# Kernel tuning notes

Measured on AMD Instinct MI355X. Metric: run time of the kernel, lower is better.

The kernel has to match this reference:

```python
import jax, jax.numpy as jnp
import numpy as np

N, F, H, G = 4096, 256, 8, 128  # atoms, filters, heads, groups
D = F // H  # head dim = 32


def setup_inputs() -> dict:
    key = jax.random.key(0)
    ks = jax.random.split(key, 12)
    x = jax.random.normal(ks[0], (N, F), dtype=jnp.float32)
    # sorted group ids in [0, G): block_diag over unique-count blocks == equality mask on sorted ids
    seg = jnp.sort(jax.random.randint(ks[1], (N,), 0, G, dtype=jnp.int32))
    elem_index = jnp.stack([jnp.arange(N, dtype=jnp.int32), seg])  # [2, N]
    s = 1.0 / np.sqrt(F)
    def lin(k):
        kw, kb = jax.random.split(k)
        return (jax.random.normal(kw, (F, F), dtype=jnp.float32) * s,
                jnp.zeros((F,), dtype=jnp.float32))
    Wq, bq = lin(ks[2]); Wk, bk = lin(ks[3]); Wv, bv = lin(ks[4])
    Wo1, bo1 = lin(ks[5]); Wo2, bo2 = lin(ks[6])
    return {"x": x, "elem_index": elem_index,
            "Wq": Wq, "bq": bq, "Wk": Wk, "bk": bk, "Wv": Wv, "bv": bv,
            "Wo1": Wo1, "bo1": bo1, "Wo2": Wo2, "bo2": bo2}


def reference(x, elem_index, Wq, bq, Wk, bk, Wv, bv, Wo1, bo1, Wo2, bo2):
    n = x.shape[0]
    # projections -> [H, N, D]
    q = (x @ Wq.T + bq).reshape(n, H, D).transpose(1, 0, 2)
    k = (x @ Wk.T + bk).reshape(n, H, D).transpose(1, 0, 2)
    v = (x @ Wv.T + bv).reshape(n, H, D).transpose(1, 0, 2)
    attn = jnp.einsum('hnd,hmd->hnm', q, k)          # [H, N, N]
    attn = jax.nn.silu(attn)                          # attn_act = activation() in source
    seg = elem_index[1]
    mask = (seg[:, None] == seg[None, :]).astype(attn.dtype)  # block-diagonal (sorted ids)
    attn = attn * mask
    out = jnp.einsum('hnm,hmd->hnd', attn, v)        # [H, N, D]
    out = out.transpose(1, 0, 2).reshape(n, F)       # [N, F]
    out = out @ Wo1.T + bo1
    out = jax.ops.segment_sum(out, seg, num_segments=G)  # scatter sum by group -> [G, F]
    out = out @ Wo2.T + bo2
    return jax.nn.silu(out)
```

## Files before the change

kernel.cpp:

```cpp
#include <hip/hip_runtime.h>
#include <math.h>

#define NATOMS 4096
#define FDIM   256
#define NHEAD  8
#define DHEAD  32
#define NGRP   128

typedef __bf16 bf16x8 __attribute__((ext_vector_type(8)));
typedef float  floatx4 __attribute__((ext_vector_type(4)));
typedef unsigned short u16x4 __attribute__((ext_vector_type(4)));

__device__ __forceinline__ float silu_f(float x) {
    return x / (1.0f + __expf(-x));
}

__device__ __forceinline__ unsigned short f2bf(float f) {
    union { float f; unsigned int u; } a;
    a.f = f;
    unsigned int r = a.u + 0x7FFF + ((a.u >> 16) & 1);
    return (unsigned short)(r >> 16);
}

__global__ __launch_bounds__(256) void prep_kernel(
    const float* __restrict__ x,
    const float* __restrict__ Wq, const float* __restrict__ Wk, const float* __restrict__ Wv,
    const float* __restrict__ bq, const float* __restrict__ bk, const float* __restrict__ bv,
    const int* __restrict__ seg,
    unsigned short* __restrict__ xb, unsigned short* __restrict__ Wb,
    float* __restrict__ b_all, int* __restrict__ off, float* __restrict__ cntf)
{
    int tid = threadIdx.x;
    unsigned int u = blockIdx.x * 256 + tid;

    if (blockIdx.x == 0 && tid < NGRP) {
        int g = tid;
        auto lb = [&](int val) {
            int lo = 0, hi = NATOMS;
            while (lo < hi) {
                int mid = (lo + hi) >> 1;
                if (seg[mid] < val) lo = mid + 1; else hi = mid;
            }
            return lo;
        };
        int a = lb(g);
        int b = lb(g + 1);
        off[g] = a;
        if (g == NGRP - 1) off[NGRP] = NATOMS;
        cntf[g] = (float)(b - a);
    }
    if (blockIdx.x == 1 && tid < 192) {
        const float* src = (tid < 64) ? bq : (tid < 128) ? bk : bv;
        int t = tid & 63;
        ((float4*)b_all)[tid] = ((const float4*)src)[t];
    }

    const unsigned int NX4 = 262144;
    const unsigned int NW4 = 16384;
    float4 fv;
    u16x4* dst;
    if (u < NX4) {
        fv = ((const float4*)x)[u];
        dst = (u16x4*)xb + u;
    } else {
        unsigned int r = u - NX4;
        unsigned int w = r / NW4;
        unsigned int i = r - w * NW4;
        const float* W = (w == 0) ? Wq : (w == 1) ? Wk : Wv;
        fv = ((const float4*)W)[i];
        dst = (u16x4*)Wb + (size_t)w * NW4 + i;
    }
    u16x4 o;
    o[0] = f2bf(fv.x); o[1] = f2bf(fv.y); o[2] = f2bf(fv.z); o[3] = f2bf(fv.w);
    *dst = o;
}

__global__ __launch_bounds__(256) void qkv_mfma(
    const unsigned short* __restrict__ xb, const unsigned short* __restrict__ Wb,
    const float* __restrict__ b_all, float* __restrict__ qkv)
{
    int tid = threadIdx.x;
    int lane = tid & 63;
    int ww = tid >> 6;
    int wrow = ww >> 1, wcol = ww & 1;
    int m_base = blockIdx.x * 64 + wrow * 32;
    int n_base = blockIdx.y * 128 + wcol * 64;

    int l15 = lane & 15;
    int quad = lane >> 4;
    int kq = quad * 8;

    floatx4 acc[2][4] = {};

    const unsigned short* arow0 = xb + (size_t)(m_base + l15) * 256 + kq;
    const unsigned short* arow1 = arow0 + 16 * 256;
    const unsigned short* brow[4];
#pragma unroll
    for (int ni = 0; ni < 4; ++ni)
        brow[ni] = Wb + (size_t)(n_base + ni * 16 + l15) * 256 + kq;

#pragma unroll
    for (int ks = 0; ks < 8; ++ks) {
        int ko = ks * 32;
        bf16x8 a0 = *(const bf16x8*)(arow0 + ko);
        bf16x8 a1 = *(const bf16x8*)(arow1 + ko);
#pragma unroll
        for (int ni = 0; ni < 4; ++ni) {
            bf16x8 b = *(const bf16x8*)(brow[ni] + ko);
            acc[0][ni] = __builtin_amdgcn_mfma_f32_16x16x32_bf16(a0, b, acc[0][ni], 0, 0, 0);
            acc[1][ni] = __builtin_amdgcn_mfma_f32_16x16x32_bf16(a1, b, acc[1][ni], 0, 0, 0);
        }
    }

#pragma unroll
    for (int mi = 0; mi < 2; ++mi) {
#pragma unroll
        for (int ni = 0; ni < 4; ++ni) {
            int col_g = n_base + ni * 16 + l15;
            int w = col_g >> 8, c = col_g & 255;
            float bias = b_all[col_g];
            float* outp = qkv + (size_t)w * (NATOMS * FDIM) + c;
#pragma unroll
            for (int r = 0; r < 4; ++r) {
                int row = m_base + mi * 16 + quad * 4 + r;
                outp[(size_t)row * FDIM] = acc[mi][ni][r] + bias;
            }
        }
    }
}

__global__ __launch_bounds__(256) void gemm_small(
    const float* __restrict__ A, const float* __restrict__ B,
    const float* __restrict__ bias, const float* __restrict__ rowScale,
    float* __restrict__ C, int M, int Ncols, int K, int act)
{
    __shared__ float As[32][36];
    __shared__ float Bs[32][36];

    int tid = threadIdx.x;
    int bm = blockIdx.y * 32;
    int bn = blockIdx.x * 32;
    int tx = tid & 15;
    int ty = tid >> 4;
    int lm = tid >> 3;
    int lk = (tid & 7) << 2;

    float acc[2][2] = {};

    for (int kt = 0; kt < K; kt += 32) {
        const float4 av = *(const float4*)(A + (size_t)(bm + lm) * K + kt + lk);
        const float4 bv = *(const float4*)(B + (size_t)(bn + lm) * K + kt + lk);
        As[lk + 0][lm] = av.x; As[lk + 1][lm] = av.y;
        As[lk + 2][lm] = av.z; As[lk + 3][lm] = av.w;
        Bs[lk + 0][lm] = bv.x; Bs[lk + 1][lm] = bv.y;
        Bs[lk + 2][lm] = bv.z; Bs[lk + 3][lm] = bv.w;
        __syncthreads();

#pragma unroll
        for (int kk = 0; kk < 32; ++kk) {
            float a0 = As[kk][ty * 2], a1 = As[kk][ty * 2 + 1];
            float c0 = Bs[kk][tx * 2], c1 = Bs[kk][tx * 2 + 1];
            acc[0][0] = fmaf(a0, c0, acc[0][0]);
            acc[0][1] = fmaf(a0, c1, acc[0][1]);
            acc[1][0] = fmaf(a1, c0, acc[1][0]);
            acc[1][1] = fmaf(a1, c1, acc[1][1]);
        }
        __syncthreads();
    }

#pragma unroll
    for (int i = 0; i < 2; ++i) {
        int m = bm + ty * 2 + i;
        float rs = rowScale ? rowScale[m] : 1.0f;
#pragma unroll
        for (int j = 0; j < 2; ++j) {
            int n = bn + tx * 2 + j;
            float vv = acc[i][j] + rs * bias[n];
            if (act) vv = silu_f(vv);
            C[(size_t)m * Ncols + n] = vv;
        }
    }
}

#define JT 32
#define IT 64

__global__ __launch_bounds__(256) void attn_kernel(
    const float* __restrict__ q, const float* __restrict__ k,
    const float* __restrict__ v, const int* __restrict__ off,
    float* __restrict__ Ysum)
{
    int g = blockIdx.x, h = blockIdx.y;
    int base = off[g];
    int end  = off[g + 1];
    base = min(max(base, 0), NATOMS);
    end  = min(max(end, base), NATOMS);
    int n = end - base;

    __shared__ float4 qt4[IT * 8];
    __shared__ float4 vt4[JT * 8];
    __shared__ float  wred[8][JT];
    __shared__ float  w[JT];
    __shared__ float  red[8][DHEAD];

    int tid = threadIdx.x;
    int jj = tid & 31;
    int iq = tid >> 5;
    int d = tid & 31;
    int r = tid >> 5;

    const float4* q4 = (const float4*)(q + (size_t)base * FDIM) + h * 8;
    const float4* k4 = (const float4*)(k + (size_t)base * FDIM) + h * 8;
    const float4* v4 = (const float4*)(v + (size_t)base * FDIM) + h * 8;

    float accY = 0.0f;

    for (int j0 = 0; j0 < n; j0 += JT) {
        int jt_n = min(JT, n - j0);
        __syncthreads();
        for (int idx = tid; idx < jt_n * 8; idx += 256)
            vt4[idx] = v4[(size_t)(j0 + (idx >> 3)) * 64 + (idx & 7)];

        float4 kr[8];
        {
            int jrow = (jj < jt_n) ? (j0 + jj) : j0;
#pragma unroll
            for (int c = 0; c < 8; ++c) kr[c] = k4[(size_t)jrow * 64 + c];
        }

        float wpart = 0.0f;
        for (int i0 = 0; i0 < n; i0 += IT) {
            int it_n = min(IT, n - i0);
            __syncthreads();
            for (int idx = tid; idx < it_n * 8; idx += 256)
                qt4[idx] = q4[(size_t)(i0 + (idx >> 3)) * 64 + (idx & 7)];
            __syncthreads();
            if (jj < jt_n) {
                for (int ii = iq; ii < it_n; ii += 8) {
                    const float4* qr = &qt4[ii * 8];
                    float s = 0.0f;
#pragma unroll
                    for (int c = 0; c < 8; ++c) {
                        float4 a = qr[c];
                        s = fmaf(a.x, kr[c].x, s);
                        s = fmaf(a.y, kr[c].y, s);
                        s = fmaf(a.z, kr[c].z, s);
                        s = fmaf(a.w, kr[c].w, s);
                    }
                    wpart += silu_f(s);
                }
            }
        }
        wred[iq][jj] = wpart;
        __syncthreads();
        if (tid < JT) {
            float s = 0.0f;
#pragma unroll
            for (int rr = 0; rr < 8; ++rr) s += wred[rr][tid];
            w[tid] = s;
        }
        __syncthreads();
        const float* vts = (const float*)vt4;
        for (int j = r; j < jt_n; j += 8)
            accY = fmaf(w[j], vts[j * 32 + d], accY);
    }

    red[r][d] = accY;
    __syncthreads();
    if (r == 0) {
        float s = 0.0f;
#pragma unroll
        for (int rr = 0; rr < 8; ++rr) s += red[rr][d];
        Ysum[(size_t)g * FDIM + h * DHEAD + d] = s;
    }
}

extern "C" void kernel_launch(void* const* d_in, const int* in_sizes, int n_in,
                              void* d_out, int out_size, void* d_ws, size_t ws_size,
                              hipStream_t stream) {
    const float* x    = (const float*)d_in[0];
    const int*   eidx = (const int*)  d_in[1];
    const float* Wq   = (const float*)d_in[2];
    const float* bq   = (const float*)d_in[3];
    const float* Wk   = (const float*)d_in[4];
    const float* bk   = (const float*)d_in[5];
    const float* Wv   = (const float*)d_in[6];
    const float* bv   = (const float*)d_in[7];
    const float* Wo1  = (const float*)d_in[8];
    const float* bo1  = (const float*)d_in[9];
    const float* Wo2  = (const float*)d_in[10];
    const float* bo2  = (const float*)d_in[11];
    float* out = (float*)d_out;

    const int* seg = eidx + NATOMS;

    const size_t NF = (size_t)NATOMS * FDIM;
    const size_t GF = (size_t)NGRP * FDIM;

    float* q     = (float*)d_ws;
    float* k     = q + NF;
    float* v     = k + NF;
    float* Ysum  = v + NF;
    float* S     = Ysum + GF;
    float* cntf  = S + GF;
    float* b_all = cntf + NGRP;
    int*   off   = (int*)(b_all + 768);
    unsigned short* xb = (unsigned short*)((float*)off + 160);
    unsigned short* Wb = xb + NF;

    prep_kernel<<<1216, 256, 0, stream>>>(x, Wq, Wk, Wv, bq, bk, bv, seg,
                                          xb, Wb, b_all, off, cntf);

    dim3 gproj(NATOMS / 64, 768 / 128);
    qkv_mfma<<<gproj, 256, 0, stream>>>(xb, Wb, b_all, q);

    dim3 gattn(NGRP, NHEAD);
    attn_kernel<<<gattn, 256, 0, stream>>>(q, k, v, off, Ysum);

    dim3 gsmall(FDIM / 32, NGRP / 32);
    gemm_small<<<gsmall, 256, 0, stream>>>(Ysum, Wo1, bo1, cntf, S, NGRP, FDIM, FDIM, 0);

    gemm_small<<<gsmall, 256, 0, stream>>>(S, Wo2, bo2, nullptr, out, NGRP, FDIM, FDIM, 1);
}
```

Before: 128.2 us.

## Fuse all stages into one persistent cooperative kernel with grid syncs

Replaces the five separate launches (prep/convert, QKV MFMA GEMM, attention, two small GEMMs) with a single cooperative kernel of 256 blocks that loops over each stage's work and uses grid.sync between stages. This removes per-launch overhead and the separate bias-gather buffer, since biases are now read directly. In exchange, attention runs as 4 serial (group, head) jobs per block instead of 1024 concurrent blocks, which lowers occupancy and latency hiding. It also adds grid-wide barrier costs, and the QKV phase spreads 384 tiles unevenly over 256 blocks.

```diff
diff --git a/kernel.cpp b/kernel.cpp
--- a/kernel.cpp
+++ b/kernel.cpp
@@ -1,11 +1,15 @@
 #include <hip/hip_runtime.h>
+#include <hip/hip_cooperative_groups.h>
 #include <math.h>
+
+namespace cg = cooperative_groups;
 
 #define NATOMS 4096
 #define FDIM   256
 #define NHEAD  8
 #define DHEAD  32
 #define NGRP   128
+#define NBLK   256
 
 typedef __bf16 bf16x8 __attribute__((ext_vector_type(8)));
 typedef float  floatx4 __attribute__((ext_vector_type(4)));
@@ -22,18 +26,91 @@
     return (unsigned short)(r >> 16);
 }
 
-__global__ __launch_bounds__(256) void prep_kernel(
-    const float* __restrict__ x,
+struct SharedMem {
+    union {
+        struct {
+            float4 qt4[64 * 8];
+            float4 vt4[32 * 8];
+            float  wred[8][32];
+            float  w[32];
+            float  red[8][32];
+        } a;
+        struct {
+            float As[32][36];
+            float Bs[32][36];
+        } g;
+    };
+};
+
+__device__ void gemm32_body(SharedMem& sm,
+                            const float* __restrict__ A, const float* __restrict__ B,
+                            const float* __restrict__ bias, const float* __restrict__ rowScale,
+                            float* __restrict__ C, int act, int blk)
+{
+    const int K = FDIM, Ncols = FDIM;
+    int tid = threadIdx.x;
+    int bm = (blk >> 3) * 32;
+    int bn = (blk & 7) * 32;
+    int tx = tid & 15;
+    int ty = tid >> 4;
+    int lm = tid >> 3;
+    int lk = (tid & 7) << 2;
+
+    float acc[2][2] = {};
+
+    for (int kt = 0; kt < K; kt += 32) {
+        const float4 av = *(const float4*)(A + (size_t)(bm + lm) * K + kt + lk);
+        const float4 bv = *(const float4*)(B + (size_t)(bn + lm) * K + kt + lk);
+        sm.g.As[lk + 0][lm] = av.x; sm.g.As[lk + 1][lm] = av.y;
+        sm.g.As[lk + 2][lm] = av.z; sm.g.As[lk + 3][lm] = av.w;
+        sm.g.Bs[lk + 0][lm] = bv.x; sm.g.Bs[lk + 1][lm] = bv.y;
+        sm.g.Bs[lk + 2][lm] = bv.z; sm.g.Bs[lk + 3][lm] = bv.w;
+        __syncthreads();
+
+#pragma unroll
+        for (int kk = 0; kk < 32; ++kk) {
+            float a0 = sm.g.As[kk][ty * 2], a1 = sm.g.As[kk][ty * 2 + 1];
+            float c0 = sm.g.Bs[kk][tx * 2], c1 = sm.g.Bs[kk][tx * 2 + 1];
+            acc[0][0] = fmaf(a0, c0, acc[0][0]);
+            acc[0][1] = fmaf(a0, c1, acc[0][1]);
+            acc[1][0] = fmaf(a1, c0, acc[1][0]);
+            acc[1][1] = fmaf(a1, c1, acc[1][1]);
+        }
+        __syncthreads();
+    }
+
+#pragma unroll
+    for (int i = 0; i < 2; ++i) {
+        int m = bm + ty * 2 + i;
+        float rs = rowScale ? rowScale[m] : 1.0f;
+#pragma unroll
+        for (int j = 0; j < 2; ++j) {
+            int n = bn + tx * 2 + j;
+            float vv = acc[i][j] + rs * bias[n];
+            if (act) vv = silu_f(vv);
+            C[(size_t)m * Ncols + n] = vv;
+        }
+    }
+}
+
+__global__ __launch_bounds__(256) void mega_kernel(
+    const float* __restrict__ x, const int* __restrict__ seg,
     const float* __restrict__ Wq, const float* __restrict__ Wk, const float* __restrict__ Wv,
     const float* __restrict__ bq, const float* __restrict__ bk, const float* __restrict__ bv,
-    const int* __restrict__ seg,
+    const float* __restrict__ Wo1, const float* __restrict__ bo1,
+    const float* __restrict__ Wo2, const float* __restrict__ bo2,
+    float* __restrict__ out,
     unsigned short* __restrict__ xb, unsigned short* __restrict__ Wb,
-    float* __restrict__ b_all, int* __restrict__ off, float* __restrict__ cntf)
+    float* __restrict__ qkv, float* __restrict__ Ysum, float* __restrict__ S,
+    float* __restrict__ cntf, int* __restrict__ off)
 {
-    int tid = threadIdx.x;
-    unsigned int u = blockIdx.x * 256 + tid;
-
-    if (blockIdx.x == 0 && tid < NGRP) {
+    cg::grid_group grid = cg::this_grid();
+    __shared__ SharedMem sm;
+
+    const int tid = threadIdx.x;
+    const int bid = blockIdx.x;
+
+    if (bid == 0 && tid < NGRP) {
         int g = tid;
         auto lb = [&](int val) {
             int lo = 0, hi = NATOMS;
@@ -49,230 +126,179 @@
         if (g == NGRP - 1) off[NGRP] = NATOMS;
         cntf[g] = (float)(b - a);
     }
-    if (blockIdx.x == 1 && tid < 192) {
-        const float* src = (tid < 64) ? bq : (tid < 128) ? bk : bv;
-        int t = tid & 63;
-        ((float4*)b_all)[tid] = ((const float4*)src)[t];
-    }
 
     const unsigned int NX4 = 262144;
     const unsigned int NW4 = 16384;
-    float4 fv;
-    u16x4* dst;
-    if (u < NX4) {
-        fv = ((const float4*)x)[u];
-        dst = (u16x4*)xb + u;
-    } else {
-        unsigned int r = u - NX4;
-        unsigned int w = r / NW4;
-        unsigned int i = r - w * NW4;
-        const float* W = (w == 0) ? Wq : (w == 1) ? Wk : Wv;
-        fv = ((const float4*)W)[i];
-        dst = (u16x4*)Wb + (size_t)w * NW4 + i;
-    }
-    u16x4 o;
-    o[0] = f2bf(fv.x); o[1] = f2bf(fv.y); o[2] = f2bf(fv.z); o[3] = f2bf(fv.w);
-    *dst = o;
-}
-
-__global__ __launch_bounds__(256) void qkv_mfma(
-    const unsigned short* __restrict__ xb, const unsigned short* __restrict__ Wb,
-    const float* __restrict__ b_all, float* __restrict__ qkv)
-{
-    int tid = threadIdx.x;
-    int lane = tid & 63;
-    int ww = tid >> 6;
-    int wrow = ww >> 1, wcol = ww & 1;
-    int m_base = blockIdx.x * 64 + wrow * 32;
-    int n_base = blockIdx.y * 128 + wcol * 64;
-
-    int l15 = lane & 15;
-    int quad = lane >> 4;
-    int kq = quad * 8;
-
-    floatx4 acc[2][4] = {};
-
-    const unsigned short* arow0 = xb + (size_t)(m_base + l15) * 256 + kq;
-    const unsigned short* arow1 = arow0 + 16 * 256;
-    const unsigned short* brow[4];
-#pragma unroll
-    for (int ni = 0; ni < 4; ++ni)
-        brow[ni] = Wb + (size_t)(n_base + ni * 16 + l15) * 256 + kq;
-
-#pragma unroll
-    for (int ks = 0; ks < 8; ++ks) {
-        int ko = ks * 32;
-        bf16x8 a0 = *(const bf16x8*)(arow0 + ko);
-        bf16x8 a1 = *(const bf16x8*)(arow1 + ko);
-#pragma unroll
-        for (int ni = 0; ni < 4; ++ni) {
-            bf16x8 b = *(const bf16x8*)(brow[ni] + ko);
-            acc[0][ni] = __builtin_amdgcn_mfma_f32_16x16x32_bf16(a0, b, acc[0][ni], 0, 0, 0);
-            acc[1][ni] = __builtin_amdgcn_mfma_f32_16x16x32_bf16(a1, b, acc[1][ni], 0, 0, 0);
-        }
-    }
-
-#pragma unroll
-    for (int mi = 0; mi < 2; ++mi) {
-#pragma unroll
-        for (int ni = 0; ni < 4; ++ni) {
-            int col_g = n_base + ni * 16 + l15;
-            int w = col_g >> 8, c = col_g & 255;
-            float bias = b_all[col_g];
-            float* outp = qkv + (size_t)w * (NATOMS * FDIM) + c;
-#pragma unroll
-            for (int r = 0; r < 4; ++r) {
-                int row = m_base + mi * 16 + quad * 4 + r;
-                outp[(size_t)row * FDIM] = acc[mi][ni][r] + bias;
-            }
-        }
-    }
-}
-
-__global__ __launch_bounds__(256) void gemm_small(
-    const float* __restrict__ A, const float* __restrict__ B,
-    const float* __restrict__ bias, const float* __restrict__ rowScale,
-    float* __restrict__ C, int M, int Ncols, int K, int act)
-{
-    __shared__ float As[32][36];
-    __shared__ float Bs[32][36];
-
-    int tid = threadIdx.x;
-    int bm = blockIdx.y * 32;
-    int bn = blockIdx.x * 32;
-    int tx = tid & 15;
-    int ty = tid >> 4;
-    int lm = tid >> 3;
-    int lk = (tid & 7) << 2;
-
-    float acc[2][2] = {};
-
-    for (int kt = 0; kt < K; kt += 32) {
-        const float4 av = *(const float4*)(A + (size_t)(bm + lm) * K + kt + lk);
-        const float4 bv = *(const float4*)(B + (size_t)(bn + lm) * K + kt + lk);
-        As[lk + 0][lm] = av.x; As[lk + 1][lm] = av.y;
-        As[lk + 2][lm] = av.z; As[lk + 3][lm] = av.w;
-        Bs[lk + 0][lm] = bv.x; Bs[lk + 1][lm] = bv.y;
-        Bs[lk + 2][lm] = bv.z; Bs[lk + 3][lm] = bv.w;
-        __syncthreads();
-
-#pragma unroll
-        for (int kk = 0; kk < 32; ++kk) {
-            float a0 = As[kk][ty * 2], a1 = As[kk][ty * 2 + 1];
-            float c0 = Bs[kk][tx * 2], c1 = Bs[kk][tx * 2 + 1];
-            acc[0][0] = fmaf(a0, c0, acc[0][0]);
-            acc[0][1] = fmaf(a0, c1, acc[0][1]);
-            acc[1][0] = fmaf(a1, c0, acc[1][0]);
-            acc[1][1] = fmaf(a1, c1, acc[1][1]);
-        }
-        __syncthreads();
-    }
-
-#pragma unroll
-    for (int i = 0; i < 2; ++i) {
-        int m = bm + ty * 2 + i;
-        float rs = rowScale ? rowScale[m] : 1.0f;
-#pragma unroll
-        for (int j = 0; j < 2; ++j) {
-            int n = bn + tx * 2 + j;
-            float vv = acc[i][j] + rs * bias[n];
-            if (act) vv = silu_f(vv);
-            C[(size_t)m * Ncols + n] = vv;
-        }
-    }
-}
-
-#define JT 32
-#define IT 64
-
-__global__ __launch_bounds__(256) void attn_kernel(
-    const float* __restrict__ q, const float* __restrict__ k,
-    const float* __restrict__ v, const int* __restrict__ off,
-    float* __restrict__ Ysum)
-{
-    int g = blockIdx.x, h = blockIdx.y;
-    int base = off[g];
-    int end  = off[g + 1];
-    base = min(max(base, 0), NATOMS);
-    end  = min(max(end, base), NATOMS);
-    int n = end - base;
-
-    __shared__ float4 qt4[IT * 8];
-    __shared__ float4 vt4[JT * 8];
-    __shared__ float  wred[8][JT];
-    __shared__ float  w[JT];
-    __shared__ float  red[8][DHEAD];
-
-    int tid = threadIdx.x;
-    int jj = tid & 31;
-    int iq = tid >> 5;
-    int d = tid & 31;
-    int r = tid >> 5;
-
-    const float4* q4 = (const float4*)(q + (size_t)base * FDIM) + h * 8;
-    const float4* k4 = (const float4*)(k + (size_t)base * FDIM) + h * 8;
-    const float4* v4 = (const float4*)(v + (size_t)base * FDIM) + h * 8;
-
-    float accY = 0.0f;
-
-    for (int j0 = 0; j0 < n; j0 += JT) {
-        int jt_n = min(JT, n - j0);
-        __syncthreads();
-        for (int idx = tid; idx < jt_n * 8; idx += 256)
-            vt4[idx] = v4[(size_t)(j0 + (idx >> 3)) * 64 + (idx & 7)];
-
-        float4 kr[8];
-        {
-            int jrow = (jj < jt_n) ? (j0 + jj) : j0;
-#pragma unroll
-            for (int c = 0; c < 8; ++c) kr[c] = k4[(size_t)jrow * 64 + c];
-        }
-
-        float wpart = 0.0f;
-        for (int i0 = 0; i0 < n; i0 += IT) {
-            int it_n = min(IT, n - i0);
+    const unsigned int NTOT = NX4 + 3 * NW4;
+    for (unsigned int u = bid * 256u + tid; u < NTOT; u += NBLK * 256u) {
+        float4 fv;
+        u16x4* dst;
+        if (u < NX4) {
+            fv = ((const float4*)x)[u];
+            dst = (u16x4*)xb + u;
+        } else {
+            unsigned int r = u - NX4;
+            unsigned int w = r / NW4;
+            unsigned int i = r - w * NW4;
+            const float* W = (w == 0) ? Wq : (w == 1) ? Wk : Wv;
+            fv = ((const float4*)W)[i];
+            dst = (u16x4*)Wb + (size_t)w * NW4 + i;
+        }
+        u16x4 o;
+        o[0] = f2bf(fv.x); o[1] = f2bf(fv.y); o[2] = f2bf(fv.z); o[3] = f2bf(fv.w);
+        *dst = o;
+    }
+    grid.sync();
+
+    {
+        int lane = tid & 63;
+        int ww = tid >> 6;
+        int wrow = ww >> 1, wcol = ww & 1;
+        int l15 = lane & 15;
+        int quad = lane >> 4;
+        int kq = quad * 8;
+
+        for (int job = bid; job < 384; job += NBLK) {
+            int tm = job & 63;
+            int tn = job >> 6;
+            int m_base = tm * 64 + wrow * 32;
+            int n_base = tn * 128 + wcol * 64;
+
+            floatx4 acc[2][4] = {};
+
+            const unsigned short* arow0 = xb + (size_t)(m_base + l15) * 256 + kq;
+            const unsigned short* arow1 = arow0 + 16 * 256;
+            const unsigned short* brow[4];
+#pragma unroll
+            for (int ni = 0; ni < 4; ++ni)
+                brow[ni] = Wb + (size_t)(n_base + ni * 16 + l15) * 256 + kq;
+
+#pragma unroll
+            for (int ks = 0; ks < 8; ++ks) {
+                int ko = ks * 32;
+                bf16x8 a0 = *(const bf16x8*)(arow0 + ko);
+                bf16x8 a1 = *(const bf16x8*)(arow1 + ko);
+#pragma unroll
+                for (int ni = 0; ni < 4; ++ni) {
+                    bf16x8 b = *(const bf16x8*)(brow[ni] + ko);
+                    acc[0][ni] = __builtin_amdgcn_mfma_f32_16x16x32_bf16(a0, b, acc[0][ni], 0, 0, 0);
+                    acc[1][ni] = __builtin_amdgcn_mfma_f32_16x16x32_bf16(a1, b, acc[1][ni], 0, 0, 0);
+                }
+            }
+
+#pragma unroll
+            for (int mi = 0; mi < 2; ++mi) {
+#pragma unroll
+                for (int ni = 0; ni < 4; ++ni) {
+                    int col_g = n_base + ni * 16 + l15;
+                    int w = col_g >> 8, c = col_g & 255;
+                    const float* bptr = (w == 0) ? bq : (w == 1) ? bk : bv;
+                    float bias = bptr[c];
+                    float* outp = qkv + (size_t)w * ((size_t)NATOMS * FDIM) + c;
+#pragma unroll
+                    for (int r = 0; r < 4; ++r) {
+                        int row = m_base + mi * 16 + quad * 4 + r;
+                        outp[(size_t)row * FDIM] = acc[mi][ni][r] + bias;
+                    }
+                }
+            }
+        }
+    }
+    grid.sync();
+
+    {
+        const float* q = qkv;
+        const float* k = qkv + (size_t)NATOMS * FDIM;
+        const float* v = qkv + 2 * (size_t)NATOMS * FDIM;
+
+        int jj = tid & 31;
+        int iq = tid >> 5;
+        int d = tid & 31;
+        int r = tid >> 5;
+
+        for (int t = 0; t < 4; ++t) {
+            int job = bid * 4 + t;
+            int g = job >> 3, h = job & 7;
+
+            int base = off[g];
+            int end  = off[g + 1];
+            base = min(max(base, 0), NATOMS);
+            end  = min(max(end, base), NATOMS);
+            int n = end - base;
+
+            const float4* q4 = (const float4*)(q + (size_t)base * FDIM) + h * 8;
+            const float4* k4 = (const float4*)(k + (size_t)base * FDIM) + h * 8;
+            const float4* v4 = (const float4*)(v + (size_t)base * FDIM) + h * 8;
+
+            float accY = 0.0f;
+
+            for (int j0 = 0; j0 < n; j0 += 32) {
+                int jt_n = min(32, n - j0);
+                __syncthreads();
+                for (int idx = tid; idx < jt_n * 8; idx += 256)
+                    sm.a.vt4[idx] = v4[(size_t)(j0 + (idx >> 3)) * 64 + (idx & 7)];
+
+                float4 kr[8];
+                {
+                    int jrow = (jj < jt_n) ? (j0 + jj) : j0;
+#pragma unroll
+                    for (int c = 0; c < 8; ++c) kr[c] = k4[(size_t)jrow * 64 + c];
+                }
+
+                float wpart = 0.0f;
+                for (int i0 = 0; i0 < n; i0 += 64) {
+                    int it_n = min(64, n - i0);
+                    __syncthreads();
+                    for (int idx = tid; idx < it_n * 8; idx += 256)
+                        sm.a.qt4[idx] = q4[(size_t)(i0 + (idx >> 3)) * 64 + (idx & 7)];
+                    __syncthreads();
+                    if (jj < jt_n) {
+                        for (int ii = iq; ii < it_n; ii += 8) {
+                            const float4* qr = &sm.a.qt4[ii * 8];
+                            float s = 0.0f;
+#pragma unroll
+                            for (int c = 0; c < 8; ++c) {
+                                float4 a = qr[c];
+                                s = fmaf(a.x, kr[c].x, s);
+                                s = fmaf(a.y, kr[c].y, s);
+                                s = fmaf(a.z, kr[c].z, s);
+                                s = fmaf(a.w, kr[c].w, s);
+                            }
+                            wpart += silu_f(s);
+                        }
+                    }
+                }
+                sm.a.wred[iq][jj] = wpart;
+                __syncthreads();
+                if (tid < 32) {
+                    float s = 0.0f;
+#pragma unroll
+                    for (int rr = 0; rr < 8; ++rr) s += sm.a.wred[rr][tid];
+                    sm.a.w[tid] = s;
+                }
+                __syncthreads();
+                const float* vts = (const float*)sm.a.vt4;
+                for (int j = r; j < jt_n; j += 8)
+                    accY = fmaf(sm.a.w[j], vts[j * 32 + d], accY);
+            }
+
+            sm.a.red[r][d] = accY;
             __syncthreads();
-            for (int idx = tid; idx < it_n * 8; idx += 256)
-                qt4[idx] = q4[(size_t)(i0 + (idx >> 3)) * 64 + (idx & 7)];
+            if (r == 0) {
+                float s = 0.0f;
+#pragma unroll
+                for (int rr = 0; rr < 8; ++rr) s += sm.a.red[rr][d];
+                Ysum[(size_t)g * FDIM + h * DHEAD + d] = s;
+            }
             __syncthreads();
-            if (jj < jt_n) {
-                for (int ii = iq; ii < it_n; ii += 8) {
-                    const float4* qr = &qt4[ii * 8];
-                    float s = 0.0f;
-#pragma unroll
-                    for (int c = 0; c < 8; ++c) {
-                        float4 a = qr[c];
-                        s = fmaf(a.x, kr[c].x, s);
-                        s = fmaf(a.y, kr[c].y, s);
-                        s = fmaf(a.z, kr[c].z, s);
-                        s = fmaf(a.w, kr[c].w, s);
-                    }
-                    wpart += silu_f(s);
-                }
-            }
-        }
-        wred[iq][jj] = wpart;
-        __syncthreads();
-        if (tid < JT) {
-            float s = 0.0f;
-#pragma unroll
-            for (int rr = 0; rr < 8; ++rr) s += wred[rr][tid];
-            w[tid] = s;
-        }
-        __syncthreads();
-        const float* vts = (const float*)vt4;
-        for (int j = r; j < jt_n; j += 8)
-            accY = fmaf(w[j], vts[j * 32 + d], accY);
-    }
-
-    red[r][d] = accY;
-    __syncthreads();
-    if (r == 0) {
-        float s = 0.0f;
-#pragma unroll
-        for (int rr = 0; rr < 8; ++rr) s += red[rr][d];
-        Ysum[(size_t)g * FDIM + h * DHEAD + d] = s;
-    }
+        }
+    }
+    grid.sync();
+
+    if (bid < 32) gemm32_body(sm, Ysum, Wo1, bo1, cntf, S, 0, bid);
+    grid.sync();
+
+    if (bid < 32) gemm32_body(sm, S, Wo2, bo2, nullptr, out, 1, bid);
 }
 
 extern "C" void kernel_launch(void* const* d_in, const int* in_sizes, int n_in,
@@ -297,28 +323,24 @@
     const size_t NF = (size_t)NATOMS * FDIM;
     const size_t GF = (size_t)NGRP * FDIM;
 
-    float* q     = (float*)d_ws;
-    float* k     = q + NF;
-    float* v     = k + NF;
-    float* Ysum  = v + NF;
+    float* qkv   = (float*)d_ws;
+    float* Ysum  = qkv + 3 * NF;
     float* S     = Ysum + GF;
     float* cntf  = S + GF;
-    float* b_all = cntf + NGRP;
-    int*   off   = (int*)(b_all + 768);
+    int*   off   = (int*)(cntf + NGRP);
     unsigned short* xb = (unsigned short*)((float*)off + 160);
     unsigned short* Wb = xb + NF;
 
-    prep_kernel<<<1216, 256, 0, stream>>>(x, Wq, Wk, Wv, bq, bk, bv, seg,
-                                          xb, Wb, b_all, off, cntf);
-
-    dim3 gproj(NATOMS / 64, 768 / 128);
-    qkv_mfma<<<gproj, 256, 0, stream>>>(xb, Wb, b_all, q);
-
-    dim3 gattn(NGRP, NHEAD);
-    attn_kernel<<<gattn, 256, 0, stream>>>(q, k, v, off, Ysum);
-
-    dim3 gsmall(FDIM / 32, NGRP / 32);
-    gemm_small<<<gsmall, 256, 0, stream>>>(Ysum, Wo1, bo1, cntf, S, NGRP, FDIM, FDIM, 0);
-
-    gemm_small<<<gsmall, 256, 0, stream>>>(S, Wo2, bo2, nullptr, out, NGRP, FDIM, FDIM, 1);
-}
+    void* args[] = {
+        (void*)&x, (void*)&seg,
+        (void*)&Wq, (void*)&Wk, (void*)&Wv,
+        (void*)&bq, (void*)&bk, (void*)&bv,
+        (void*)&Wo1, (void*)&bo1, (void*)&Wo2, (void*)&bo2,
+        (void*)&out,
+        (void*)&xb, (void*)&Wb,
+        (void*)&qkv, (void*)&Ysum, (void*)&S,
+        (void*)&cntf, (void*)&off
+    };
+    hipLaunchCooperativeKernel((const void*)mega_kernel,
+                               dim3(NBLK), dim3(256), args, 0, stream);
+}
```

After: 269.7 us. 2.1x slower.

## Fuse prep into QKV GEMM and precompose output weights Wo2·Wo1

Applied to the files above, without the earlier changes.

Drops the separate bf16 conversion kernel: the QKV MFMA GEMM now reads fp32 x and weights directly and converts them in registers. The same launch also precomputes A2 = Wo2·Wo1 and c1 = Wo2·bo1, plus the group offsets. The two tail GEMMs collapse into one Ysum·A2ᵀ + cnt·c1 + bo2 with SiLU. This cuts launches from five to three and removes the intermediate bf16 buffers, but re-reads fp32 inputs at twice the bytes and reassociates the tail arithmetic.

```diff
diff --git a/kernel.cpp b/kernel.cpp
--- a/kernel.cpp
+++ b/kernel.cpp
@@ -9,185 +9,161 @@
 
 typedef __bf16 bf16x8 __attribute__((ext_vector_type(8)));
 typedef float  floatx4 __attribute__((ext_vector_type(4)));
-typedef unsigned short u16x4 __attribute__((ext_vector_type(4)));
 
 __device__ __forceinline__ float silu_f(float x) {
     return x / (1.0f + __expf(-x));
 }
 
-__device__ __forceinline__ unsigned short f2bf(float f) {
-    union { float f; unsigned int u; } a;
-    a.f = f;
-    unsigned int r = a.u + 0x7FFF + ((a.u >> 16) & 1);
-    return (unsigned short)(r >> 16);
-}
-
-__global__ __launch_bounds__(256) void prep_kernel(
-    const float* __restrict__ x,
+__device__ __forceinline__ bf16x8 cvt8(const float* __restrict__ p) {
+    float4 f0 = *(const float4*)p;
+    float4 f1 = *(const float4*)(p + 4);
+    bf16x8 r;
+    r[0] = (__bf16)f0.x; r[1] = (__bf16)f0.y; r[2] = (__bf16)f0.z; r[3] = (__bf16)f0.w;
+    r[4] = (__bf16)f1.x; r[5] = (__bf16)f1.y; r[6] = (__bf16)f1.z; r[7] = (__bf16)f1.w;
+    return r;
+}
+
+__global__ __launch_bounds__(256) void k1_qkv_a2(
+    const float* __restrict__ x, const int* __restrict__ seg,
     const float* __restrict__ Wq, const float* __restrict__ Wk, const float* __restrict__ Wv,
     const float* __restrict__ bq, const float* __restrict__ bk, const float* __restrict__ bv,
-    const int* __restrict__ seg,
-    unsigned short* __restrict__ xb, unsigned short* __restrict__ Wb,
-    float* __restrict__ b_all, int* __restrict__ off, float* __restrict__ cntf)
+    const float* __restrict__ Wo1, const float* __restrict__ bo1,
+    const float* __restrict__ Wo2,
+    float* __restrict__ qkv, float* __restrict__ A2, float* __restrict__ c1,
+    float* __restrict__ cntf, int* __restrict__ off)
 {
-    int tid = threadIdx.x;
-    unsigned int u = blockIdx.x * 256 + tid;
-
-    if (blockIdx.x == 0 && tid < NGRP) {
-        int g = tid;
-        auto lb = [&](int val) {
-            int lo = 0, hi = NATOMS;
-            while (lo < hi) {
-                int mid = (lo + hi) >> 1;
-                if (seg[mid] < val) lo = mid + 1; else hi = mid;
+    __shared__ float As[32][33];
+    __shared__ float Bs[32][33];
+
+    const int tid = threadIdx.x;
+    const int bid = blockIdx.x;
+
+    if (bid < 512) {
+        int lane = tid & 63;
+        int ww = tid >> 6;
+        int wrow = ww >> 1, wcol = ww & 1;
+        int tm = bid & 63;
+        int tn = bid >> 6;
+        int m_base = tm * 64 + wrow * 32;
+        int n_base = tn * 96 + wcol * 48;
+
+        int l15 = lane & 15;
+        int quad = lane >> 4;
+        int kq = quad * 8;
+
+        floatx4 acc[2][3] = {};
+
+        const float* arow0 = x + (size_t)(m_base + l15) * 256 + kq;
+        const float* arow1 = arow0 + 16 * 256;
+        const float* brow[3];
+        const float* bias[3];
+#pragma unroll
+        for (int ni = 0; ni < 3; ++ni) {
+            int col = n_base + ni * 16 + l15;
+            int w = col >> 8, c = col & 255;
+            const float* W = (w == 0) ? Wq : (w == 1) ? Wk : Wv;
+            brow[ni] = W + (size_t)c * 256 + kq;
+            bias[ni] = ((w == 0) ? bq : (w == 1) ? bk : bv) + c;
+        }
+
+#pragma unroll
+        for (int ks = 0; ks < 8; ++ks) {
+            int ko = ks * 32;
+            bf16x8 a0 = cvt8(arow0 + ko);
+            bf16x8 a1 = cvt8(arow1 + ko);
+#pragma unroll
+            for (int ni = 0; ni < 3; ++ni) {
+                bf16x8 b = cvt8(brow[ni] + ko);
+                acc[0][ni] = __builtin_amdgcn_mfma_f32_16x16x32_bf16(a0, b, acc[0][ni], 0, 0, 0);
+                acc[1][ni] = __builtin_amdgcn_mfma_f32_16x16x32_bf16(a1, b, acc[1][ni], 0, 0, 0);
             }
-            return lo;
-        };
-        int a = lb(g);
-        int b = lb(g + 1);
-        off[g] = a;
-        if (g == NGRP - 1) off[NGRP] = NATOMS;
-        cntf[g] = (float)(b - a);
+        }
+
+#pragma unroll
+        for (int mi = 0; mi < 2; ++mi) {
+#pragma unroll
+            for (int ni = 0; ni < 3; ++ni) {
+                int col = n_base + ni * 16 + l15;
+                int w = col >> 8, c = col & 255;
+                float bb = *bias[ni];
+                float* outp = qkv + (size_t)w * ((size_t)NATOMS * FDIM) + c;
+#pragma unroll
+                for (int r = 0; r < 4; ++r) {
+                    int row = m_base + mi * 16 + quad * 4 + r;
+                    outp[(size_t)row * FDIM] = acc[mi][ni][r] + bb;
+                }
+            }
+        }
+    } else if (bid < 576) {
+        int t = bid - 512;
+        int i0 = (t >> 3) * 32;
+        int j0 = (t & 7) * 32;
+        int tx = tid & 15;
+        int ty = tid >> 4;
+        int lm = tid >> 3;
+        int lk = (tid & 7) << 2;
+
+        float acc[2][2] = {};
+
+        for (int kt = 0; kt < 256; kt += 32) {
+            const float4 av = *(const float4*)(Wo2 + (size_t)(i0 + lm) * 256 + kt + lk);
+            const float4 bv = *(const float4*)(Wo1 + (size_t)(kt + lm) * 256 + j0 + lk);
+            As[lk + 0][lm] = av.x; As[lk + 1][lm] = av.y;
+            As[lk + 2][lm] = av.z; As[lk + 3][lm] = av.w;
+            Bs[lm][lk + 0] = bv.x; Bs[lm][lk + 1] = bv.y;
+            Bs[lm][lk + 2] = bv.z; Bs[lm][lk + 3] = bv.w;
+            __syncthreads();
+
+#pragma unroll
+            for (int kk = 0; kk < 32; ++kk) {
+                float a0 = As[kk][ty * 2], a1 = As[kk][ty * 2 + 1];
+                float b0 = Bs[kk][tx * 2], b1 = Bs[kk][tx * 2 + 1];
+                acc[0][0] = fmaf(a0, b0, acc[0][0]);
+                acc[0][1] = fmaf(a0, b1, acc[0][1]);
+                acc[1][0] = fmaf(a1, b0, acc[1][0]);
+                acc[1][1] = fmaf(a1, b1, acc[1][1]);
+            }
+            __syncthreads();
+        }
+
+#pragma unroll
+        for (int i = 0; i < 2; ++i)
+#pragma unroll
+            for (int j = 0; j < 2; ++j)
+                A2[(size_t)(i0 + ty * 2 + i) * 256 + j0 + tx * 2 + j] = acc[i][j];
+    } else {
+        if (tid < NGRP) {
+            int g = tid;
+            auto lb = [&](int val) {
+                int lo = 0, hi = NATOMS;
+                while (lo < hi) {
+                    int mid = (lo + hi) >> 1;
+                    if (seg[mid] < val) lo = mid + 1; else hi = mid;
+                }
+                return lo;
+            };
+            int a = lb(g);
+            int b = lb(g + 1);
+            off[g] = a;
+            if (g == NGRP - 1) off[NGRP] = NATOMS;
+            cntf[g] = (float)(b - a);
+        }
+        int lane = tid & 63;
+        int ww = tid >> 6;
+        float4 b4 = ((const float4*)bo1)[lane];
+        for (int i = ww * 64; i < ww * 64 + 64; ++i) {
+            float4 wv = ((const float4*)(Wo2 + (size_t)i * 256))[lane];
+            float p = wv.x * b4.x + wv.y * b4.y + wv.z * b4.z + wv.w * b4.w;
+#pragma unroll
+            for (int m = 32; m >= 1; m >>= 1)
+                p += __shfl_xor(p, m, 64);
+            if (lane == 0) c1[i] = p;
+        }
     }
-    if (blockIdx.x == 1 && tid < 192) {
-        const float* src = (tid < 64) ? bq : (tid < 128) ? bk : bv;
-        int t = tid & 63;
-        ((float4*)b_all)[tid] = ((const float4*)src)[t];
-    }
-
-    const unsigned int NX4 = 262144;
-    const unsigned int NW4 = 16384;
-    float4 fv;
-    u16x4* dst;
-    if (u < NX4) {
-        fv = ((const float4*)x)[u];
-        dst = (u16x4*)xb + u;
-    } else {
-        unsigned int r = u - NX4;
-        unsigned int w = r / NW4;
-        unsigned int i = r - w * NW4;
-        const float* W = (w == 0) ? Wq : (w == 1) ? Wk : Wv;
-        fv = ((const float4*)W)[i];
-        dst = (u16x4*)Wb + (size_t)w * NW4 + i;
-    }
-    u16x4 o;
-    o[0] = f2bf(fv.x); o[1] = f2bf(fv.y); o[2] = f2bf(fv.z); o[3] = f2bf(fv.w);
-    *dst = o;
-}
-
-__global__ __launch_bounds__(256) void qkv_mfma(
-    const unsigned short* __restrict__ xb, const unsigned short* __restrict__ Wb,
-    const float* __restrict__ b_all, float* __restrict__ qkv)
-{
-    int tid = threadIdx.x;
-    int lane = tid & 63;
-    int ww = tid >> 6;
-    int wrow = ww >> 1, wcol = ww & 1;
-    int m_base = blockIdx.x * 64 + wrow * 32;
-    int n_base = blockIdx.y * 128 + wcol * 64;
-
-    int l15 = lane & 15;
-    int quad = lane >> 4;
-    int kq = quad * 8;
-
-    floatx4 acc[2][4] = {};
-
-    const unsigned short* arow0 = xb + (size_t)(m_base + l15) * 256 + kq;
-    const unsigned short* arow1 = arow0 + 16 * 256;
-    const unsigned short* brow[4];
-#pragma unroll
-    for (int ni = 0; ni < 4; ++ni)
-        brow[ni] = Wb + (size_t)(n_base + ni * 16 + l15) * 256 + kq;
-
-#pragma unroll
-    for (int ks = 0; ks < 8; ++ks) {
-        int ko = ks * 32;
-        bf16x8 a0 = *(const bf16x8*)(arow0 + ko);
-        bf16x8 a1 = *(const bf16x8*)(arow1 + ko);
-#pragma unroll
-        for (int ni = 0; ni < 4; ++ni) {
-            bf16x8 b = *(const bf16x8*)(brow[ni] + ko);
-            acc[0][ni] = __builtin_amdgcn_mfma_f32_16x16x32_bf16(a0, b, acc[0][ni], 0, 0, 0);
-            acc[1][ni] = __builtin_amdgcn_mfma_f32_16x16x32_bf16(a1, b, acc[1][ni], 0, 0, 0);
-        }
-    }
-
-#pragma unroll
-    for (int mi = 0; mi < 2; ++mi) {
-#pragma unroll
-        for (int ni = 0; ni < 4; ++ni) {
-            int col_g = n_base + ni * 16 + l15;
-            int w = col_g >> 8, c = col_g & 255;
-            float bias = b_all[col_g];
-            float* outp = qkv + (size_t)w * (NATOMS * FDIM) + c;
-#pragma unroll
-            for (int r = 0; r < 4; ++r) {
-                int row = m_base + mi * 16 + quad * 4 + r;
-                outp[(size_t)row * FDIM] = acc[mi][ni][r] + bias;
-            }
-        }
-    }
-}
-
-__global__ __launch_bounds__(256) void gemm_small(
-    const float* __restrict__ A, const float* __restrict__ B,
-    const float* __restrict__ bias, const float* __restrict__ rowScale,
-    float* __restrict__ C, int M, int Ncols, int K, int act)
-{
-    __shared__ float As[32][36];
-    __shared__ float Bs[32][36];
-
-    int tid = threadIdx.x;
-    int bm = blockIdx.y * 32;
-    int bn = blockIdx.x * 32;
-    int tx = tid & 15;
-    int ty = tid >> 4;
-    int lm = tid >> 3;
-    int lk = (tid & 7) << 2;
-
-    float acc[2][2] = {};
-
-    for (int kt = 0; kt < K; kt += 32) {
-        const float4 av = *(const float4*)(A + (size_t)(bm + lm) * K + kt + lk);
-        const float4 bv = *(const float4*)(B + (size_t)(bn + lm) * K + kt + lk);
-        As[lk + 0][lm] = av.x; As[lk + 1][lm] = av.y;
-        As[lk + 2][lm] = av.z; As[lk + 3][lm] = av.w;
-        Bs[lk + 0][lm] = bv.x; Bs[lk + 1][lm] = bv.y;
-        Bs[lk + 2][lm] = bv.z; Bs[lk + 3][lm] = bv.w;
-        __syncthreads();
-
-#pragma unroll
-        for (int kk = 0; kk < 32; ++kk) {
-            float a0 = As[kk][ty * 2], a1 = As[kk][ty * 2 + 1];
-            float c0 = Bs[kk][tx * 2], c1 = Bs[kk][tx * 2 + 1];
-            acc[0][0] = fmaf(a0, c0, acc[0][0]);
-            acc[0][1] = fmaf(a0, c1, acc[0][1]);
-            acc[1][0] = fmaf(a1, c0, acc[1][0]);
-            acc[1][1] = fmaf(a1, c1, acc[1][1]);
-        }
-        __syncthreads();
-    }
-
-#pragma unroll
-    for (int i = 0; i < 2; ++i) {
-        int m = bm + ty * 2 + i;
-        float rs = rowScale ? rowScale[m] : 1.0f;
-#pragma unroll
-        for (int j = 0; j < 2; ++j) {
-            int n = bn + tx * 2 + j;
-            float vv = acc[i][j] + rs * bias[n];
-            if (act) vv = silu_f(vv);
-            C[(size_t)m * Ncols + n] = vv;
-        }
-    }
-}
-
-#define JT 32
-#define IT 64
+}
 
 __global__ __launch_bounds__(256) void attn_kernel(
-    const float* __restrict__ q, const float* __restrict__ k,
-    const float* __restrict__ v, const int* __restrict__ off,
+    const float* __restrict__ qkv, const int* __restrict__ off,
     float* __restrict__ Ysum)
 {
     int g = blockIdx.x, h = blockIdx.y;
@@ -197,11 +173,11 @@
     end  = min(max(end, base), NATOMS);
     int n = end - base;
 
-    __shared__ float4 qt4[IT * 8];
-    __shared__ float4 vt4[JT * 8];
-    __shared__ float  wred[8][JT];
-    __shared__ float  w[JT];
-    __shared__ float  red[8][DHEAD];
+    __shared__ float4 qt4[64 * 8];
+    __shared__ float4 vt4[32 * 8];
+    __shared__ float  wred[8][32];
+    __shared__ float  w[32];
+    __shared__ float  red[8][32];
 
     int tid = threadIdx.x;
     int jj = tid & 31;
@@ -209,14 +185,18 @@
     int d = tid & 31;
     int r = tid >> 5;
 
+    const float* q = qkv;
+    const float* k = qkv + (size_t)NATOMS * FDIM;
+    const float* v = qkv + 2 * (size_t)NATOMS * FDIM;
+
     const float4* q4 = (const float4*)(q + (size_t)base * FDIM) + h * 8;
     const float4* k4 = (const float4*)(k + (size_t)base * FDIM) + h * 8;
     const float4* v4 = (const float4*)(v + (size_t)base * FDIM) + h * 8;
 
     float accY = 0.0f;
 
-    for (int j0 = 0; j0 < n; j0 += JT) {
-        int jt_n = min(JT, n - j0);
+    for (int j0 = 0; j0 < n; j0 += 32) {
+        int jt_n = min(32, n - j0);
         __syncthreads();
         for (int idx = tid; idx < jt_n * 8; idx += 256)
             vt4[idx] = v4[(size_t)(j0 + (idx >> 3)) * 64 + (idx & 7)];
@@ -229,8 +209,8 @@
         }
 
         float wpart = 0.0f;
-        for (int i0 = 0; i0 < n; i0 += IT) {
-            int it_n = min(IT, n - i0);
+        for (int i0 = 0; i0 < n; i0 += 64) {
+            int it_n = min(64, n - i0);
             __syncthreads();
             for (int idx = tid; idx < it_n * 8; idx += 256)
                 qt4[idx] = q4[(size_t)(i0 + (idx >> 3)) * 64 + (idx & 7)];
@@ -253,7 +233,7 @@
         }
         wred[iq][jj] = wpart;
         __syncthreads();
-        if (tid < JT) {
+        if (tid < 32) {
             float s = 0.0f;
 #pragma unroll
             for (int rr = 0; rr < 8; ++rr) s += wred[rr][tid];
@@ -273,6 +253,55 @@
         for (int rr = 0; rr < 8; ++rr) s += red[rr][d];
         Ysum[(size_t)g * FDIM + h * DHEAD + d] = s;
     }
+}
+
+__global__ __launch_bounds__(256) void k3_tail(
+    const float* __restrict__ Ysum, const float* __restrict__ A2,
+    const float* __restrict__ c1, const float* __restrict__ bo2,
+    const float* __restrict__ cntf, float* __restrict__ out)
+{
+    __shared__ float As[32][17];
+    __shared__ float Bs[32][33];
+
+    int tid = threadIdx.x;
+    int bm = (blockIdx.x >> 3) * 16;
+    int bn = (blockIdx.x & 7) * 32;
+    int tx = tid & 15;
+    int ty = tid >> 4;
+
+    float acc0 = 0.0f, acc1 = 0.0f;
+
+    for (int kt = 0; kt < 256; kt += 32) {
+        if (tid < 128) {
+            int row = tid >> 3, kq = (tid & 7) << 2;
+            const float4 av = *(const float4*)(Ysum + (size_t)(bm + row) * 256 + kt + kq);
+            As[kq + 0][row] = av.x; As[kq + 1][row] = av.y;
+            As[kq + 2][row] = av.z; As[kq + 3][row] = av.w;
+        }
+        {
+            int row = tid >> 3, kq = (tid & 7) << 2;
+            const float4 bv = *(const float4*)(A2 + (size_t)(bn + row) * 256 + kt + kq);
+            Bs[kq + 0][row] = bv.x; Bs[kq + 1][row] = bv.y;
+            Bs[kq + 2][row] = bv.z; Bs[kq + 3][row] = bv.w;
+        }
+        __syncthreads();
+
+#pragma unroll
+        for (int kk = 0; kk < 32; ++kk) {
+            float a = As[kk][ty];
+            acc0 = fmaf(a, Bs[kk][tx * 2], acc0);
+            acc1 = fmaf(a, Bs[kk][tx * 2 + 1], acc1);
+        }
+        __syncthreads();
+    }
+
+    int m = bm + ty;
+    float cnt = cntf[m];
+    int n0 = bn + tx * 2;
+    float v0 = silu_f(acc0 + cnt * c1[n0] + bo2[n0]);
+    float v1 = silu_f(acc1 + cnt * c1[n0 + 1] + bo2[n0 + 1]);
+    out[(size_t)m * 256 + n0] = v0;
+    out[(size_t)m * 256 + n0 + 1] = v1;
 }
 
 extern "C" void kernel_launch(void* const* d_in, const int* in_sizes, int n_in,
@@ -297,28 +326,18 @@
     const size_t NF = (size_t)NATOMS * FDIM;
     const size_t GF = (size_t)NGRP * FDIM;
 
-    float* q     = (float*)d_ws;
-    float* k     = q + NF;
-    float* v     = k + NF;
-    float* Ysum  = v + NF;
-    float* S     = Ysum + GF;
-    float* cntf  = S + GF;
-    float* b_all = cntf + NGRP;
-    int*   off   = (int*)(b_all + 768);
-    unsigned short* xb = (unsigned short*)((float*)off + 160);
-    unsigned short* Wb = xb + NF;
-
-    prep_kernel<<<1216, 256, 0, stream>>>(x, Wq, Wk, Wv, bq, bk, bv, seg,
-                                          xb, Wb, b_all, off, cntf);
-
-    dim3 gproj(NATOMS / 64, 768 / 128);
-    qkv_mfma<<<gproj, 256, 0, stream>>>(xb, Wb, b_all, q);
+    float* qkv  = (float*)d_ws;
+    float* Ysum = qkv + 3 * NF;
+    float* A2   = Ysum + GF;
+    float* c1   = A2 + 256 * 256;
+    float* cntf = c1 + 256;
+    int*   off  = (int*)(cntf + NGRP);
+
+    k1_qkv_a2<<<577, 256, 0, stream>>>(x, seg, Wq, Wk, Wv, bq, bk, bv,
+                                       Wo1, bo1, Wo2, qkv, A2, c1, cntf, off);
 
     dim3 gattn(NGRP, NHEAD);
-    attn_kernel<<<gattn, 256, 0, stream>>>(q, k, v, off, Ysum);
-
-    dim3 gsmall(FDIM / 32, NGRP / 32);
-    gemm_small<<<gsmall, 256, 0, stream>>>(Ysum, Wo1, bo1, cntf, S, NGRP, FDIM, FDIM, 0);
-
-    gemm_small<<<gsmall, 256, 0, stream>>>(S, Wo2, bo2, nullptr, out, NGRP, FDIM, FDIM, 1);
-}
+    attn_kernel<<<gattn, 256, 0, stream>>>(qkv, off, Ysum);
+
+    k3_tail<<<64, 256, 0, stream>>>(Ysum, A2, c1, bo2, cntf, out);
+}
```

Result: slower. 153.2 us (+19.5%).
